# Performance work log

Measured on AMD Instinct MI355X. Metric: run time of the kernel, lower is better.

Reference implementation:

```python
import jax, jax.numpy as jnp
import numpy as np

N = 100000      # nodes
E = 800000      # edges
P = 200000      # number of subgraph permutations
L = 16          # lrp_length
D = 64          # lrp_out_dim (== lrp_in_dim)
PL = P * L
LEN_SEQ = 4     # int(sqrt(L))
NUM_BOND = 4


def setup_inputs() -> dict:
    key = jax.random.key(0)
    ks = jax.random.split(key, 16)
    inp = {}
    inp["nfeat"] = jax.random.normal(ks[0], (N, D), jnp.float32)
    inp["degs"] = jax.random.uniform(ks[1], (N,), jnp.float32) * 8.0 + 1.0
    inp["n2p_val"] = jnp.ones((PL,), jnp.float32)
    inp["e2p_val"] = jnp.ones((PL,), jnp.float32)
    inp["pool_val"] = jax.random.uniform(ks[2], (P,), jnp.float32)
    inp["weights"] = jax.random.normal(ks[3], (D, D, L), jnp.float32)
    inp["bias"] = jnp.zeros((1, D), jnp.float32)
    inp["w_deg0"] = jax.random.normal(ks[4], (2 * D, LEN_SEQ), jnp.float32) * 0.3
    inp["b_deg0"] = jnp.zeros((2 * D,), jnp.float32)
    inp["w_deg1"] = jax.random.normal(ks[5], (D, 2 * D), jnp.float32) * 0.1
    inp["b_deg1"] = jnp.zeros((D,), jnp.float32)
    inp["w_lin"] = jax.random.normal(ks[6], (D, D), jnp.float32) * 0.1
    inp["b_lin"] = jnp.zeros((D,), jnp.float32)
    inp["bond_emb"] = jax.random.normal(ks[7], (NUM_BOND, D), jnp.float32)
    inp["edge_feat_idx"] = jax.random.randint(ks[8], (E,), 0, NUM_BOND, jnp.int32)
    inp["n2p_row"] = jnp.arange(PL, dtype=jnp.int32)
    inp["n2p_col"] = jax.random.randint(ks[9], (PL,), 0, N, jnp.int32)
    inp["e2p_row"] = jnp.arange(PL, dtype=jnp.int32)
    inp["e2p_col"] = jax.random.randint(ks[10], (PL,), 0, E, jnp.int32)
    inp["pool_row"] = jax.random.randint(ks[11], (P,), 0, N, jnp.int32)
    inp["pool_col"] = jnp.arange(P, dtype=jnp.int32)
    return inp


def _spmm(row, col, val, x, m):
    # COO spmm: out[r] = sum_{nnz with row==r} val * x[col]
    return jax.ops.segment_sum(val[:, None] * x[col], row, num_segments=m)


def reference(nfeat, degs, n2p_val, e2p_val, pool_val, weights, bias,
              w_deg0, b_deg0, w_deg1, b_deg1, w_lin, b_lin, bond_emb,
              edge_feat_idx, n2p_row, n2p_col, e2p_row, e2p_col,
              pool_row, pool_col):
    n = nfeat.shape[0]
    pl = n2p_row.shape[0]
    d = weights.shape[0]
    l = weights.shape[2]
    p = pl // l
    len_seq = int(round(l ** 0.5))

    efeat = bond_emb[edge_feat_idx]                                  # [E, D]
    perm = _spmm(n2p_row, n2p_col, n2p_val, nfeat, pl) \
         + _spmm(e2p_row, e2p_col, e2p_val, efeat, pl)               # [P*L, D]
    deg_perm = _spmm(n2p_row, n2p_col, n2p_val, degs[:, None], pl)   # [P*L, 1]

    x = perm.reshape(p, l, d)                                        # [P, L, D]
    deg_sel = deg_perm.reshape(p, l)[:, ::len_seq + 1]               # [P, len_seq]

    h = jnp.einsum('pab,bca->pc', x, weights) + bias                 # [P, D]
    h = jax.nn.relu(h) @ w_lin.T + b_lin                             # linear(relu(.))

    g = jax.nn.relu(deg_sel @ w_deg0.T + b_deg0) @ w_deg1.T + b_deg1  # [P, D]
    h = h * g

    out = _spmm(pool_row, pool_col, pool_val, h, n)                  # [N, D]
    return out
```

## Files before the change

### kernel.cpp

```cpp
#include <hip/hip_runtime.h>
#include <hip/hip_bf16.h>

typedef __attribute__((ext_vector_type(8))) __bf16 bf16x8;
typedef __attribute__((ext_vector_type(4))) float floatx4;
typedef __attribute__((ext_vector_type(2))) float floatx2;
typedef __attribute__((ext_vector_type(4))) int intx4;
typedef __attribute__((ext_vector_type(2))) unsigned uintx2;

constexpr int N_NODES = 100000;
constexpr int P_PERM  = 200000;

constexpr size_t W2F_OFF  = 0;
constexpr size_t WLF_OFF  = 131072;
constexpr size_t WD1F_OFF = 139264;
constexpr size_t BE_OFF   = 155648;
constexpr size_t NF8_OFF  = 3355648;
constexpr size_t WS_NEED_FULL = 3355648 + (size_t)N_NODES * 64;

__device__ inline unsigned pack_fp8x4(float x0, float x1, float x2, float x3) {
  int w = __builtin_amdgcn_cvt_pk_fp8_f32(x0, x1, 0, false);
  w = __builtin_amdgcn_cvt_pk_fp8_f32(x2, x3, w, true);
  return (unsigned)w;
}
__device__ inline floatx2 unpk_fp8_lo(unsigned w) {
  return __builtin_amdgcn_cvt_pk_f32_fp8((int)w, false);
}
__device__ inline floatx2 unpk_fp8_hi(unsigned w) {
  return __builtin_amdgcn_cvt_pk_f32_fp8((int)w, true);
}

__global__ void zero_out_kernel(float4* __restrict__ out) {
  out[blockIdx.x * 256 + threadIdx.x] = make_float4(0.f, 0.f, 0.f, 0.f);
}

__global__ void prep_all_kernel(const float* __restrict__ weights,
                                const float* __restrict__ w_lin,
                                const float* __restrict__ w_deg1,
                                const float* __restrict__ nfeat,
                                const int* __restrict__ e2p_col,
                                const int* __restrict__ edge_feat_idx,
                                __bf16* __restrict__ ws_bf) {
  int b = blockIdx.x;
  int t = threadIdx.x;
  if (b < 304) {
    int i = b * 256 + t;
    if (i < 65536) {
      int j = i & 7, l = (i >> 3) & 63, ct = (i >> 9) & 3, ks = (i >> 11) & 1, a = i >> 12;
      int k = ks * 32 + (l >> 4) * 8 + j;
      int c = ct * 16 + (l & 15);
      ws_bf[W2F_OFF / 2 + i] = (__bf16)weights[k * 1024 + c * 16 + a];
    } else if (i < 65536 + 4096) {
      int i2 = i - 65536;
      int j = i2 & 7, l = (i2 >> 3) & 63, ct = (i2 >> 9) & 3, ks = (i2 >> 11) & 1;
      int k = ks * 32 + (l >> 4) * 8 + j;
      int c = ct * 16 + (l & 15);
      ws_bf[WLF_OFF / 2 + i2] = (__bf16)w_lin[c * 64 + k];
    } else if (i < 65536 + 4096 + 8192) {
      int i3 = i - 65536 - 4096;
      int j = i3 & 7, l = (i3 >> 3) & 63, ct = (i3 >> 9) & 3, ks = (i3 >> 11) & 3;
      int k = ks * 32 + (l >> 4) * 8 + j;
      int c = ct * 16 + (l & 15);
      ws_bf[WD1F_OFF / 2 + i3] = (__bf16)w_deg1[c * 128 + k];
    }
  } else if (b < 3429) {
    int i = (b - 304) * 256 + t;
    if (i < N_NODES * 8) {
      float4 a = *(const float4*)(nfeat + (size_t)i * 8);
      float4 c = *(const float4*)(nfeat + (size_t)i * 8 + 4);
      uintx2 o;
      o.x = pack_fp8x4(a.x, a.y, a.z, a.w);
      o.y = pack_fp8x4(c.x, c.y, c.z, c.w);
      *(uintx2*)((char*)ws_bf + NF8_OFF + (size_t)i * 8) = o;
    }
  } else {
    int i = (b - 3429) * 256 + t;
    if (i < P_PERM * 4) {
      int4 ec = ((const int4*)e2p_col)[i];
      unsigned v = (unsigned)(edge_feat_idx[ec.x] & 0xff)
                 | ((unsigned)(edge_feat_idx[ec.y] & 0xff) << 8)
                 | ((unsigned)(edge_feat_idx[ec.z] & 0xff) << 16)
                 | ((unsigned)(edge_feat_idx[ec.w] & 0xff) << 24);
      ((unsigned*)((char*)ws_bf + BE_OFF))[i] = v;
    }
  }
}

template <bool BF16FEAT>
__global__ __launch_bounds__(256, 4) void lrp_mfma_kernel(
    const float* __restrict__ nfeat,
    const float* __restrict__ degs,
    const float* __restrict__ n2p_val,
    const float* __restrict__ e2p_val,
    const float* __restrict__ pool_val,
    const float* __restrict__ bias,
    const float* __restrict__ w_deg0,
    const float* __restrict__ b_deg0,
    const float* __restrict__ b_deg1,
    const float* __restrict__ b_lin,
    const float* __restrict__ bond_emb,
    const int* __restrict__ n2p_col,
    const int* __restrict__ pool_row,
    const __bf16* __restrict__ ws_bf,
    float* __restrict__ out) {
  __shared__ __align__(16) char shbig[32768];
  __bf16 (* const hs)[2][16][72] = (__bf16(*)[2][16][72])shbig;
  __shared__ __align__(16) __bf16 sbond[4][72];
  __shared__ __align__(16) float swdeg0[128][4];
  __shared__ float sbd0[128];
  __shared__ float sbias[64];
  __shared__ float sblin[64];
  __shared__ float sbd1[64];

  const int t = threadIdx.x;
  const int w = t >> 6;
  const int l = t & 63;
  const int m = l & 15;
  const int q = l >> 4;
  const int pbase = blockIdx.x * 128 + w * 32;
  int pb[2]  = {pbase, pbase + 16};
  bool valid[2];
  int pbc[2];
  #pragma unroll
  for (int pt = 0; pt < 2; ++pt) {
    valid[pt] = pb[pt] < P_PERM;
    pbc[pt] = valid[pt] ? pb[pt] : (P_PERM - 16);
  }

  if (t < 256) sbond[t >> 6][t & 63] = (__bf16)bond_emb[t];
  if (t < 128) {
    *(float4*)&swdeg0[t][0] = *(const float4*)(w_deg0 + t * 4);
    sbd0[t] = b_deg0[t];
  } else if (t < 192) {
    int c = t - 128;
    sbias[c] = bias[c]; sblin[c] = b_lin[c]; sbd1[c] = b_deg1[c];
  }

  const unsigned char* __restrict__ nf8 = (const unsigned char*)ws_bf + NF8_OFF;
  const bf16x8* __restrict__ WLv  = (const bf16x8*)(ws_bf + WLF_OFF / 2);
  const bf16x8* __restrict__ WD1v = (const bf16x8*)(ws_bf + WD1F_OFF / 2);
  const unsigned* __restrict__ bep = (const unsigned*)((const char*)ws_bf + BE_OFF);
  const char* __restrict__ W2bytes = (const char*)ws_bf + W2F_OFF;

  intx4 nvx[2], evx[2], ncx[2];
  int bex[2];
  #pragma unroll
  for (int pt = 0; pt < 2; ++pt) {
    size_t rb = (size_t)pbc[pt] * 16;
    nvx[pt] = *(const intx4*)(n2p_val + rb + 4 * l);
    evx[pt] = *(const intx4*)(e2p_val + rb + 4 * l);
    ncx[pt] = *(const intx4*)(n2p_col + rb + 4 * l);
    bex[pt] = (int)bep[(size_t)pbc[pt] * 4 + l];
  }
  const int selbase = m * 16;

  auto stage4 = [&](int period) {
    #pragma unroll
    for (int c = 0; c < 4; ++c) {
      #pragma unroll
      for (int j = 0; j < 2; ++j) {
        const char* g = W2bytes + (size_t)(period * 4 + c) * 8192 +
                        (w * 2 + j) * 1024 + l * 16;
        char* lds = &shbig[c * 8192 + (w * 2 + j) * 1024];
        __builtin_amdgcn_global_load_lds(
            (const __attribute__((address_space(1))) unsigned*)g,
            (__attribute__((address_space(3))) unsigned*)lds, 16, 0, 0);
      }
    }
  };
  auto gath = [&](int nc, uintx2* g) {
    #pragma unroll
    for (int ks = 0; ks < 2; ++ks) {
      if (BF16FEAT) {
        g[ks] = *(const uintx2*)(nf8 + (size_t)nc * 64 + ks * 32 + q * 8);
      } else {
        int k0 = ks * 32 + q * 8;
        float4 n0 = *(const float4*)(nfeat + (size_t)nc * 64 + k0);
        float4 n1 = *(const float4*)(nfeat + (size_t)nc * 64 + k0 + 4);
        uintx2 o;
        o.x = pack_fp8x4(n0.x, n0.y, n0.z, n0.w);
        o.y = pack_fp8x4(n1.x, n1.y, n1.z, n1.w);
        g[ks] = o;
      }
    }
  };

  floatx4 acc[2][4] = {};
  float dsnv[2][4];
  int dsnc[2][4];
  float nv0[2], ev0[2];
  int nc0[2], be0[2];
  uintx2 g_cur[2][2], g_nxt[2][2];

  #pragma unroll
  for (int pt = 0; pt < 2; ++pt) {
    nv0[pt] = __int_as_float(__builtin_amdgcn_ds_bpermute(selbase, nvx[pt][0]));
    ev0[pt] = __int_as_float(__builtin_amdgcn_ds_bpermute(selbase, evx[pt][0]));
    nc0[pt] = __builtin_amdgcn_ds_bpermute(selbase, ncx[pt][0]);
    be0[pt] = (__builtin_amdgcn_ds_bpermute(selbase, bex[pt])) & 0xff;
    gath(nc0[pt], g_cur[pt]);
  }
  stage4(0);
  __syncthreads();

  #pragma unroll
  for (int a = 0; a < 16; ++a) {
    const int sub = a & 3;
    float nv1[2], ev1[2];
    int nc1[2], be1[2];
    if (a < 15) {
      const int an = a + 1;
      const int sel1 = selbase + (an >> 2) * 4;
      const int sl = an & 3;
      #pragma unroll
      for (int pt = 0; pt < 2; ++pt) {
        nv1[pt] = __int_as_float(__builtin_amdgcn_ds_bpermute(sel1, nvx[pt][sl]));
        ev1[pt] = __int_as_float(__builtin_amdgcn_ds_bpermute(sel1, evx[pt][sl]));
        nc1[pt] = __builtin_amdgcn_ds_bpermute(sel1, ncx[pt][sl]);
        be1[pt] = (__builtin_amdgcn_ds_bpermute(sel1, bex[pt]) >> (sl * 8)) & 0xff;
      }
      #pragma unroll
      for (int pt = 0; pt < 2; ++pt) gath(nc1[pt], g_nxt[pt]);
    }

    bf16x8 afv[2][2];
    #pragma unroll
    for (int pt = 0; pt < 2; ++pt) {
      #pragma unroll
      for (int ks = 0; ks < 2; ++ks) {
        bf16x8 eb = *(const bf16x8*)&sbond[be0[pt]][ks * 32 + q * 8];
        uintx2 gw = g_cur[pt][ks];
        floatx2 x01 = unpk_fp8_lo(gw.x);
        floatx2 x23 = unpk_fp8_hi(gw.x);
        floatx2 x45 = unpk_fp8_lo(gw.y);
        floatx2 x67 = unpk_fp8_hi(gw.y);
        float xs[8] = {x01.x, x01.y, x23.x, x23.y, x45.x, x45.y, x67.x, x67.y};
        bf16x8 af;
        #pragma unroll
        for (int j = 0; j < 8; ++j)
          af[j] = (__bf16)fmaf(nv0[pt], xs[j], ev0[pt] * (float)eb[j]);
        afv[pt][ks] = af;
      }
    }
    #pragma unroll
    for (int ks = 0; ks < 2; ++ks)
      #pragma unroll
      for (int ct = 0; ct < 4; ++ct) {
        bf16x8 frag = *(const bf16x8*)&shbig[sub * 8192 + ((ks * 4 + ct) * 64 + l) * 16];
        acc[0][ct] = __builtin_amdgcn_mfma_f32_16x16x32_bf16(afv[0][ks], frag, acc[0][ct], 0, 0, 0);
        acc[1][ct] = __builtin_amdgcn_mfma_f32_16x16x32_bf16(afv[1][ks], frag, acc[1][ct], 0, 0, 0);
      }

    if (a == 0 || a == 5 || a == 10 || a == 15) {
      const int jj = a / 5;
      #pragma unroll
      for (int pt = 0; pt < 2; ++pt) {
        dsnv[pt][jj] = nv0[pt];
        dsnc[pt][jj] = nc0[pt];
      }
    }

    if (a < 15 && sub == 3) {
      __syncthreads();
      stage4((a + 1) >> 2);
      __syncthreads();
    }

    if (a < 15) {
      #pragma unroll
      for (int pt = 0; pt < 2; ++pt) {
        nv0[pt] = nv1[pt]; ev0[pt] = ev1[pt]; nc0[pt] = nc1[pt]; be0[pt] = be1[pt];
        g_cur[pt][0] = g_nxt[pt][0]; g_cur[pt][1] = g_nxt[pt][1];
      }
    }
  }

  float dsreg[2][4];
  #pragma unroll
  for (int pt = 0; pt < 2; ++pt)
    #pragma unroll
    for (int jj = 0; jj < 4; ++jj)
      dsreg[pt][jj] = dsnv[pt][jj] * degs[dsnc[pt][jj]];

  __syncthreads();

  floatx4 acc2[2][4] = {};
  {
    #pragma unroll
    for (int pt = 0; pt < 2; ++pt)
      #pragma unroll
      for (int ct = 0; ct < 4; ++ct) {
        float bv = sbias[ct * 16 + m];
        #pragma unroll
        for (int rr = 0; rr < 4; ++rr)
          hs[w][pt][q * 4 + rr][ct * 16 + m] =
              (__bf16)fmaxf(acc[pt][ct][rr] + bv, 0.0f);
      }
    #pragma unroll
    for (int pt = 0; pt < 2; ++pt)
      #pragma unroll
      for (int ks = 0; ks < 2; ++ks) {
        bf16x8 af2 = *(const bf16x8*)&hs[w][pt][m][ks * 32 + q * 8];
        #pragma unroll
        for (int ct = 0; ct < 4; ++ct) {
          bf16x8 frag = WLv[(ks * 4 + ct) * 64 + l];
          acc2[pt][ct] = __builtin_amdgcn_mfma_f32_16x16x32_bf16(af2, frag, acc2[pt][ct], 0, 0, 0);
        }
      }
  }

  floatx4 gacc[2][4] = {};
  #pragma unroll
  for (int ks = 0; ks < 4; ++ks) {
    const int k0 = ks * 32 + q * 8;
    bf16x8 af[2];
    #pragma unroll
    for (int j = 0; j < 8; ++j) {
      int k = k0 + j;
      float4 wr = *(const float4*)&swdeg0[k][0];
      float bk = sbd0[k];
      #pragma unroll
      for (int pt = 0; pt < 2; ++pt) {
        float v = bk;
        v = fmaf(dsreg[pt][0], wr.x, v);
        v = fmaf(dsreg[pt][1], wr.y, v);
        v = fmaf(dsreg[pt][2], wr.z, v);
        v = fmaf(dsreg[pt][3], wr.w, v);
        af[pt][j] = (__bf16)fmaxf(v, 0.0f);
      }
    }
    #pragma unroll
    for (int ct = 0; ct < 4; ++ct) {
      bf16x8 frag = WD1v[(ks * 4 + ct) * 64 + l];
      gacc[0][ct] = __builtin_amdgcn_mfma_f32_16x16x32_bf16(af[0], frag, gacc[0][ct], 0, 0, 0);
      gacc[1][ct] = __builtin_amdgcn_mfma_f32_16x16x32_bf16(af[1], frag, gacc[1][ct], 0, 0, 0);
    }
  }

  #pragma unroll
  for (int pt = 0; pt < 2; ++pt) {
    if (!valid[pt]) continue;
    intx4   pr4 = *(const intx4*)(pool_row + pb[pt] + q * 4);
    floatx4 pv4 = *(const floatx4*)(pool_val + pb[pt] + q * 4);
    #pragma unroll
    for (int rr = 0; rr < 4; ++rr) {
      float* orow = out + (size_t)pr4[rr] * 64;
      float pv = pv4[rr];
      #pragma unroll
      for (int ct = 0; ct < 4; ++ct) {
        float h2 = (acc2[pt][ct][rr] + sblin[ct * 16 + m]) *
                   (gacc[pt][ct][rr] + sbd1[ct * 16 + m]);
        atomicAdd(orow + ct * 16 + m, pv * h2);
      }
    }
  }
}

extern "C" void kernel_launch(void* const* d_in, const int* in_sizes, int n_in,
                              void* d_out, int out_size, void* d_ws, size_t ws_size,
                              hipStream_t stream) {
  const float* nfeat    = (const float*)d_in[0];
  const float* degs     = (const float*)d_in[1];
  const float* n2p_val  = (const float*)d_in[2];
  const float* e2p_val  = (const float*)d_in[3];
  const float* pool_val = (const float*)d_in[4];
  const float* weights  = (const float*)d_in[5];
  const float* bias     = (const float*)d_in[6];
  const float* w_deg0   = (const float*)d_in[7];
  const float* b_deg0   = (const float*)d_in[8];
  const float* w_deg1   = (const float*)d_in[9];
  const float* b_deg1   = (const float*)d_in[10];
  const float* w_lin    = (const float*)d_in[11];
  const float* b_lin    = (const float*)d_in[12];
  const float* bond_emb = (const float*)d_in[13];
  const int* edge_feat_idx = (const int*)d_in[14];
  const int* n2p_col    = (const int*)d_in[16];
  const int* e2p_col    = (const int*)d_in[18];
  const int* pool_row   = (const int*)d_in[19];

  float* out = (float*)d_out;
  __bf16* ws_bf = (__bf16*)d_ws;

  zero_out_kernel<<<6250, 256, 0, stream>>>((float4*)out);
  prep_all_kernel<<<6554, 256, 0, stream>>>(weights, w_lin, w_deg1, nfeat,
                                            e2p_col, edge_feat_idx, ws_bf);

  int grid = (P_PERM + 127) / 128;
  if (ws_size >= WS_NEED_FULL) {
    lrp_mfma_kernel<true><<<grid, 256, 0, stream>>>(
        nfeat, degs, n2p_val, e2p_val, pool_val, bias, w_deg0, b_deg0,
        b_deg1, b_lin, bond_emb, n2p_col, pool_row, ws_bf, out);
  } else {
    lrp_mfma_kernel<false><<<grid, 256, 0, stream>>>(
        nfeat, degs, n2p_val, e2p_val, pool_val, bias, w_deg0, b_deg0,
        b_deg1, b_lin, bond_emb, n2p_col, pool_row, ws_bf, out);
  }
}
```

Measured before the change: 286.6 us.

## Deepen gather prefetch to two steps ahead and fold zeroing into prep kernel

The main kernel now prefetches node-feature gathers two iterations ahead using a three-slot register ring, instead of one, so more gather latency can be hidden behind the MFMA work. Separately, the output-zeroing kernel is merged into the prep kernel as extra blocks, removing one kernel launch. The deeper prefetch raises register pressure under launch bounds of four blocks per SM, which could cause spills or lower occupancy.

```diff
diff --git a/kernel.cpp b/kernel.cpp
--- a/kernel.cpp
+++ b/kernel.cpp
@@ -29,11 +29,8 @@
   return __builtin_amdgcn_cvt_pk_f32_fp8((int)w, true);
 }
 
-__global__ void zero_out_kernel(float4* __restrict__ out) {
-  out[blockIdx.x * 256 + threadIdx.x] = make_float4(0.f, 0.f, 0.f, 0.f);
-}
-
-__global__ void prep_all_kernel(const float* __restrict__ weights,
+__global__ void prep_all_kernel(float4* __restrict__ out,
+                                const float* __restrict__ weights,
                                 const float* __restrict__ w_lin,
                                 const float* __restrict__ w_deg1,
                                 const float* __restrict__ nfeat,
@@ -42,8 +39,10 @@
                                 __bf16* __restrict__ ws_bf) {
   int b = blockIdx.x;
   int t = threadIdx.x;
-  if (b < 304) {
-    int i = b * 256 + t;
+  if (b < 6250) {
+    out[b * 256 + t] = make_float4(0.f, 0.f, 0.f, 0.f);
+  } else if (b < 6554) {
+    int i = (b - 6250) * 256 + t;
     if (i < 65536) {
       int j = i & 7, l = (i >> 3) & 63, ct = (i >> 9) & 3, ks = (i >> 11) & 1, a = i >> 12;
       int k = ks * 32 + (l >> 4) * 8 + j;
@@ -62,8 +61,8 @@
       int c = ct * 16 + (l & 15);
       ws_bf[WD1F_OFF / 2 + i3] = (__bf16)w_deg1[c * 128 + k];
     }
-  } else if (b < 3429) {
-    int i = (b - 304) * 256 + t;
+  } else if (b < 9679) {
+    int i = (b - 6554) * 256 + t;
     if (i < N_NODES * 8) {
       float4 a = *(const float4*)(nfeat + (size_t)i * 8);
       float4 c = *(const float4*)(nfeat + (size_t)i * 8 + 4);
@@ -73,7 +72,7 @@
       *(uintx2*)((char*)ws_bf + NF8_OFF + (size_t)i * 8) = o;
     }
   } else {
-    int i = (b - 3429) * 256 + t;
+    int i = (b - 9679) * 256 + t;
     if (i < P_PERM * 4) {
       int4 ec = ((const int4*)e2p_col)[i];
       unsigned v = (unsigned)(edge_feat_idx[ec.x] & 0xff)
@@ -187,9 +186,9 @@
   floatx4 acc[2][4] = {};
   float dsnv[2][4];
   int dsnc[2][4];
-  float nv0[2], ev0[2];
-  int nc0[2], be0[2];
-  uintx2 g_cur[2][2], g_nxt[2][2];
+  float nv0[2], ev0[2], nv1[2], ev1[2];
+  int nc0[2], be0[2], nc1[2], be1[2];
+  uintx2 g[3][2][2];
 
   #pragma unroll
   for (int pt = 0; pt < 2; ++pt) {
@@ -197,7 +196,12 @@
     ev0[pt] = __int_as_float(__builtin_amdgcn_ds_bpermute(selbase, evx[pt][0]));
     nc0[pt] = __builtin_amdgcn_ds_bpermute(selbase, ncx[pt][0]);
     be0[pt] = (__builtin_amdgcn_ds_bpermute(selbase, bex[pt])) & 0xff;
-    gath(nc0[pt], g_cur[pt]);
+    gath(nc0[pt], g[0][pt]);
+    nv1[pt] = __int_as_float(__builtin_amdgcn_ds_bpermute(selbase, nvx[pt][1]));
+    ev1[pt] = __int_as_float(__builtin_amdgcn_ds_bpermute(selbase, evx[pt][1]));
+    nc1[pt] = __builtin_amdgcn_ds_bpermute(selbase, ncx[pt][1]);
+    be1[pt] = (__builtin_amdgcn_ds_bpermute(selbase, bex[pt]) >> 8) & 0xff;
+    gath(nc1[pt], g[1][pt]);
   }
   stage4(0);
   __syncthreads();
@@ -205,21 +209,23 @@
   #pragma unroll
   for (int a = 0; a < 16; ++a) {
     const int sub = a & 3;
-    float nv1[2], ev1[2];
-    int nc1[2], be1[2];
-    if (a < 15) {
-      const int an = a + 1;
-      const int sel1 = selbase + (an >> 2) * 4;
-      const int sl = an & 3;
+    const int gcur = a % 3;
+    const int gwr  = (a + 2) % 3;
+    float nv2[2], ev2[2];
+    int nc2[2], be2[2];
+    if (a < 14) {
+      const int an2 = a + 2;
+      const int sel2 = selbase + (an2 >> 2) * 4;
+      const int sl2 = an2 & 3;
       #pragma unroll
       for (int pt = 0; pt < 2; ++pt) {
-        nv1[pt] = __int_as_float(__builtin_amdgcn_ds_bpermute(sel1, nvx[pt][sl]));
-        ev1[pt] = __int_as_float(__builtin_amdgcn_ds_bpermute(sel1, evx[pt][sl]));
-        nc1[pt] = __builtin_amdgcn_ds_bpermute(sel1, ncx[pt][sl]);
-        be1[pt] = (__builtin_amdgcn_ds_bpermute(sel1, bex[pt]) >> (sl * 8)) & 0xff;
-      }
-      #pragma unroll
-      for (int pt = 0; pt < 2; ++pt) gath(nc1[pt], g_nxt[pt]);
+        nv2[pt] = __int_as_float(__builtin_amdgcn_ds_bpermute(sel2, nvx[pt][sl2]));
+        ev2[pt] = __int_as_float(__builtin_amdgcn_ds_bpermute(sel2, evx[pt][sl2]));
+        nc2[pt] = __builtin_amdgcn_ds_bpermute(sel2, ncx[pt][sl2]);
+        be2[pt] = (__builtin_amdgcn_ds_bpermute(sel2, bex[pt]) >> (sl2 * 8)) & 0xff;
+      }
+      #pragma unroll
+      for (int pt = 0; pt < 2; ++pt) gath(nc2[pt], g[gwr][pt]);
     }
 
     bf16x8 afv[2][2];
@@ -228,7 +234,7 @@
       #pragma unroll
       for (int ks = 0; ks < 2; ++ks) {
         bf16x8 eb = *(const bf16x8*)&sbond[be0[pt]][ks * 32 + q * 8];
-        uintx2 gw = g_cur[pt][ks];
+        uintx2 gw = g[gcur][pt][ks];
         floatx2 x01 = unpk_fp8_lo(gw.x);
         floatx2 x23 = unpk_fp8_hi(gw.x);
         floatx2 x45 = unpk_fp8_lo(gw.y);
@@ -269,7 +275,12 @@
       #pragma unroll
       for (int pt = 0; pt < 2; ++pt) {
         nv0[pt] = nv1[pt]; ev0[pt] = ev1[pt]; nc0[pt] = nc1[pt]; be0[pt] = be1[pt];
-        g_cur[pt][0] = g_nxt[pt][0]; g_cur[pt][1] = g_nxt[pt][1];
+      }
+    }
+    if (a < 14) {
+      #pragma unroll
+      for (int pt = 0; pt < 2; ++pt) {
+        nv1[pt] = nv2[pt]; ev1[pt] = ev2[pt]; nc1[pt] = nc2[pt]; be1[pt] = be2[pt];
       }
     }
   }
@@ -380,9 +391,9 @@
   float* out = (float*)d_out;
   __bf16* ws_bf = (__bf16*)d_ws;
 
-  zero_out_kernel<<<6250, 256, 0, stream>>>((float4*)out);
-  prep_all_kernel<<<6554, 256, 0, stream>>>(weights, w_lin, w_deg1, nfeat,
-                                            e2p_col, edge_feat_idx, ws_bf);
+  prep_all_kernel<<<12804, 256, 0, stream>>>((float4*)out, weights, w_lin,
+                                             w_deg1, nfeat, e2p_col,
+                                             edge_feat_idx, ws_bf);
 
   int grid = (P_PERM + 127) / 128;
   if (ws_size >= WS_NEED_FULL) {
```

Measured after the change: 276.8 us. 3.4% less time.
